# Kernel optimization log

Measured on AMD Instinct MI355X. Metric: run time of the kernel, lower is better.

The kernel has to match this reference:

```python
import jax, jax.numpy as jnp
import numpy as np


def setup_inputs() -> dict:
    key = jax.random.key(0)
    k1, _ = jax.random.split(key)
    x = jax.random.normal(k1, (8, 128, 56, 56), dtype=jnp.float32)
    gamma = jnp.array(0.5, dtype=jnp.float32)  # learned scalar (init gamma=0.5)
    return {"x": x, "gamma": gamma}


def reference(x, gamma):
    # conv=False path: query/key/value convs are Identity, so Q=K=V=x flattened.
    B, C, H, W = x.shape
    N = H * W
    v = x.reshape(B, C, N)                          # [B, C, N]
    # energy[b, i, j] = sum_c x[b, c, i] * x[b, c, j]  (Q^T K)
    energy = jnp.einsum('bci,bcj->bij', v, v)       # [B, N, N]
    # multiplicative mask: zero out the diagonal BEFORE softmax (not -inf)
    mask = 1.0 - jnp.eye(N, dtype=energy.dtype)
    attention = jax.nn.softmax(energy * mask, axis=-1)  # [B, N, N]
    # out = bmm(V, attention): out[b, c, j] = sum_i v[b, c, i] * attention[b, i, j]
    out = jnp.einsum('bci,bij->bcj', v, attention)  # [B, C, N]
    out = jax.nn.relu(out).reshape(B, C, H, W)
    y = gamma * out + x
    return (y, out, x, gamma)
```

## Files before the change

kernel.cpp:

```cpp
#include <hip/hip_runtime.h>
#include <math.h>

#define Bb 8
#define Cc 128
#define Nn 3136
#define Np 3200
#define NT 50
#define Mm (Bb*Cc*Nn)
#define PADV 72
#define L2E 1.44269504088896340736f
#define C44 (44.0f * L2E)

#define XT2B (NT*16*64*8)
#define XC2B (NT*8*128*8)

typedef unsigned short u16;
typedef unsigned int   u32;
typedef __attribute__((ext_vector_type(8)))  u16      u16x8;
typedef __attribute__((ext_vector_type(8)))  _Float16 f16x8;
typedef __attribute__((ext_vector_type(4)))  _Float16 f16x4;
typedef __attribute__((ext_vector_type(4)))  float    f32x4;
typedef __attribute__((ext_vector_type(16))) float    f32x16;

__device__ __forceinline__ float exp2fast(float x) {
#if __has_builtin(__builtin_amdgcn_exp2f)
    return __builtin_amdgcn_exp2f(x);
#else
    float r; asm("v_exp_f32 %0, %1" : "=v"(r) : "v"(x)); return r;
#endif
}

__global__ __launch_bounds__(256) void prep_kernel(const float* __restrict__ x,
                                                   const float* __restrict__ gamma_p,
                                                   float* __restrict__ out,
                                                   u16* __restrict__ xt2,
                                                   u16* __restrict__ xc2,
                                                   float* __restrict__ row_d) {
    const int bx = blockIdx.x;
    const int b = bx / 50, nblk = bx % 50;
    const int t = threadIdx.x;

    if (nblk == 49) {
        const u16x8 z8 = {0, 0, 0, 0, 0, 0, 0, 0};
        u16* dt = xt2 + ((size_t)b * NT + 49) * (16 * 64 * 8);
        u16* dc = xc2 + ((size_t)b * NT + 49) * (8 * 128 * 8);
        #pragma unroll
        for (int it = 0; it < 4; ++it) {
            *(u16x8*)&dt[(it * 256 + t) * 8] = z8;
            *(u16x8*)&dc[(it * 256 + t) * 8] = z8;
        }
        if (t < 64) row_d[b * Np + Nn + t] = 1.0f;
        return;
    }

    __shared__ float lx[Cc][65];
    const int n0 = nblk * 64;

    #pragma unroll 8
    for (int r = 0; r < 32; ++r) {
        const int c = r * 4 + (t >> 6);
        const int g = (b * Cc + c) * Nn + n0 + (t & 63);
        lx[c][t & 63] = x[g];
    }
    __syncthreads();

    {
        const int nl = t & 63, cseg = t >> 6;
        u16x8 hv[4];
        #pragma unroll
        for (int cc = 0; cc < 32; ++cc) {
            const _Float16 hh = (_Float16)lx[cseg * 32 + cc][nl];
            hv[cc >> 3][cc & 7] = __builtin_bit_cast(u16, hh);
        }
        u16* base = xt2 + (((size_t)(b * NT + nblk) * 16 + cseg * 4) * 64 + nl) * 8;
        #pragma unroll
        for (int k = 0; k < 4; ++k) *(u16x8*)&base[k * (64 * 8)] = hv[k];
    }
    {
        const int c = t >> 1, half = t & 1;
        u16x8 hv[4];
        #pragma unroll
        for (int k = 0; k < 32; ++k) {
            const _Float16 hh = (_Float16)lx[c][half * 32 + k];
            hv[k >> 3][k & 7] = __builtin_bit_cast(u16, hh);
        }
        u16* base = xc2 + (((size_t)(b * NT + nblk) * 8 + half * 4) * 128 + c) * 8;
        #pragma unroll
        for (int k = 0; k < 4; ++k) *(u16x8*)&base[k * (128 * 8)] = hv[k];
    }
    if (bx == 0 && t == 0) out[(size_t)3 * Mm] = gamma_p[0];
}

__global__ __launch_bounds__(256, 5) void stats_kernel(const u16* __restrict__ xt2,
                                                       float* __restrict__ row_d) {
    const int bx = blockIdx.x;
    const int b = bx & 7, rem = bx >> 3;
    const int i0t = rem >> 3, jq = rem & 7;
    const int t = threadIdx.x;
    const int w = t >> 6, l = t & 63, lane = l & 31, h = l >> 5;
    const int igrp = w & 1, jsub = w >> 1;
    const u16* __restrict__ xb = xt2 + (size_t)b * XT2B;

    f16x8 Bf[8];
    const int irow = igrp * 32 + lane;
    #pragma unroll
    for (int kk = 0; kk < 8; ++kk)
        Bf[kk] = *(const f16x8*)&xb[(((size_t)i0t * 16 + 2 * kk + h) * 64 + irow) * 8];

    const int jt0 = jq * 6 + (jq < 2 ? jq : 2);
    const int jcnt = 6 + (jq < 2 ? 1 : 0);
    const int jrow = jsub * 32 + lane;

    float sa = 0.f, sb = 0.f;
    for (int jt = jt0; jt < jt0 + jcnt; ++jt) {
        const u16* ab = &xb[((size_t)jt * 16 * 64 + jrow) * 8];
        f32x16 ea, eb;
        #pragma unroll
        for (int r = 0; r < 16; ++r) { ea[r] = 0.f; eb[r] = 0.f; }
        __builtin_amdgcn_s_setprio(1);
        #pragma unroll
        for (int kk = 0; kk < 4; ++kk) {
            const f16x8 A0 = *(const f16x8*)&ab[(4 * kk + h) * 512];
            const f16x8 A1 = *(const f16x8*)&ab[(4 * kk + 2 + h) * 512];
            ea = __builtin_amdgcn_mfma_f32_32x32x16_f16(A0, Bf[2 * kk],     ea, 0, 0, 0);
            eb = __builtin_amdgcn_mfma_f32_32x32x16_f16(A1, Bf[2 * kk + 1], eb, 0, 0, 0);
        }
        __builtin_amdgcn_s_setprio(0);

        if (jt == i0t) {
            const bool dsub = (jsub == igrp);
            #pragma unroll
            for (int r = 0; r < 16; ++r) {
                const int mrow = (r & 3) + 8 * (r >> 2) + 4 * h;
                float v = ea[r] + eb[r];
                if (dsub && mrow == lane) v = 0.f;
                const float e = exp2fast(fmaf(v, L2E, -C44));
                if (r & 1) sb += e; else sa += e;
            }
        } else {
            #pragma unroll
            for (int r = 0; r < 16; ++r) {
                const float e = exp2fast(fmaf(ea[r] + eb[r], L2E, -C44));
                if (r & 1) sb += e; else sa += e;
            }
        }
    }
    float ssum = sa + sb;
    ssum += __shfl_xor(ssum, 32, 64);
    if (h == 0) atomicAdd(&row_d[b * Np + i0t * 64 + igrp * 32 + lane], ssum);
}

__global__ __launch_bounds__(256) void conv_kernel(float* __restrict__ row_d) {
    const int i = blockIdx.x * 256 + threadIdx.x;
    row_d[i] = C44 + __log2f(row_d[i]);
}

__global__ __launch_bounds__(256, 3) void out_kernel(const u16* __restrict__ xt2,
                                                     const u16* __restrict__ xc2,
                                                     const float* __restrict__ row_c,
                                                     float* __restrict__ out) {
    __shared__ u16 s_pt[2][64 * PADV];

    const int bx = blockIdx.x;
    const int b = bx & 7, rem = bx >> 3;
    const int j0t = rem >> 1, ih = rem & 1;
    const int ti0 = ih * 25, ti1 = ti0 + 25;
    const int t = threadIdx.x;
    const int w = t >> 6, l = t & 63, lane = l & 31, h = l >> 5;
    const int isub = w & 1, jgrp = w >> 1;
    const int jg = w & 1,  cp = w >> 1;
    const u16* __restrict__ xtb = xt2 + (size_t)b * XT2B;
    const u16* __restrict__ xcb = xc2 + (size_t)b * XC2B;

    f16x8 Bj[8];
    const int jrow = jgrp * 32 + lane;
    #pragma unroll
    for (int kk = 0; kk < 8; ++kk)
        Bj[kk] = *(const f16x8*)&xtb[(((size_t)j0t * 16 + 2 * kk + h) * 64 + jrow) * 8];

    f32x16 oa, ob;
    #pragma unroll
    for (int r = 0; r < 16; ++r) { oa[r] = 0.f; ob[r] = 0.f; }

    const int arow = isub * 32 + lane;
    const int ptbase = (jgrp * 32 + lane) * PADV + isub * 32;
    const int pbrow = (jg * 32 + lane) * PADV + h * 8;

    f16x8 Ac[8];
    {
        const u16* ab = &xtb[((size_t)ti0 * 16 * 64 + arow) * 8];
        #pragma unroll
        for (int kk = 0; kk < 8; ++kk)
            Ac[kk] = *(const f16x8*)&ab[(2 * kk + h) * 512];
    }

    for (int ti = ti0; ti < ti1; ++ti) {
        const int tn = (ti + 1 < ti1) ? ti + 1 : ti;
        f16x8 An[8];
        const u16* abn = &xtb[((size_t)tn * 16 * 64 + arow) * 8];
        #pragma unroll
        for (int kk = 0; kk < 8; ++kk)
            An[kk] = *(const f16x8*)&abn[(2 * kk + h) * 512];

        f32x16 ea;
        #pragma unroll
        for (int r = 0; r < 16; ++r) ea[r] = 0.f;
        #pragma unroll
        for (int kk = 0; kk < 8; ++kk)
            ea = __builtin_amdgcn_mfma_f32_32x32x16_f16(Ac[kk], Bj[kk], ea, 0, 0, 0);

        u16* pt = &s_pt[ti & 1][0];
        const float* cbase = &row_c[b * Np + ti * 64 + isub * 32];
        if (ti == j0t) {
            const bool dsub = (isub == jgrp);
            #pragma unroll
            for (int qq = 0; qq < 4; ++qq) {
                const f32x4 cv = *(const f32x4*)&cbase[qq * 8 + h * 4];
                f16x4 pv;
                #pragma unroll
                for (int r = 0; r < 4; ++r) {
                    const int m = qq * 8 + h * 4 + r;
                    float v = ea[qq * 4 + r];
                    if (dsub && m == lane) v = 0.f;
                    pv[r] = (_Float16)exp2fast(fmaf(v, L2E, -cv[r]));
                }
                *(f16x4*)&pt[ptbase + qq * 8 + h * 4] = pv;
            }
        } else {
            #pragma unroll
            for (int qq = 0; qq < 4; ++qq) {
                const f32x4 cv = *(const f32x4*)&cbase[qq * 8 + h * 4];
                f16x4 pv;
                #pragma unroll
                for (int r = 0; r < 4; ++r)
                    pv[r] = (_Float16)exp2fast(fmaf(ea[qq * 4 + r], L2E, -cv[r]));
                *(f16x4*)&pt[ptbase + qq * 8 + h * 4] = pv;
            }
        }

        f16x8 Av[4][2];
        const u16* vb = &xcb[((size_t)ti * 8 * 128 + cp * 64 + lane) * 8];
        #pragma unroll
        for (int kk = 0; kk < 4; ++kk) {
            Av[kk][0] = *(const f16x8*)&vb[((2 * kk + h) * 128) * 8];
            Av[kk][1] = *(const f16x8*)&vb[((2 * kk + h) * 128 + 32) * 8];
        }
        __syncthreads();

        #pragma unroll
        for (int kk = 0; kk < 4; ++kk) {
            const f16x8 Bp = *(const f16x8*)&pt[pbrow + kk * 16];
            oa = __builtin_amdgcn_mfma_f32_32x32x16_f16(Av[kk][0], Bp, oa, 0, 0, 0);
            ob = __builtin_amdgcn_mfma_f32_32x32x16_f16(Av[kk][1], Bp, ob, 0, 0, 0);
        }

        #pragma unroll
        for (int kk = 0; kk < 8; ++kk) Ac[kk] = An[kk];
    }

    #pragma unroll
    for (int r = 0; r < 16; ++r) {
        const int mrow = (r & 3) + 8 * (r >> 2) + 4 * h;
        const int jj = j0t * 64 + jg * 32 + lane;
        {
            const int c = cp * 64 + mrow;
            const size_t pos = (size_t)(b * Cc + c) * Nn + jj;
            out[(size_t)ih * Mm + pos] = oa[r];
        }
        {
            const int c = cp * 64 + 32 + mrow;
            const size_t pos = (size_t)(b * Cc + c) * Nn + jj;
            out[(size_t)ih * Mm + pos] = ob[r];
        }
    }
}

__global__ __launch_bounds__(256) void finish_kernel(const float* __restrict__ x,
                                                     const float* __restrict__ gamma_p,
                                                     float* __restrict__ out) {
    const float gamma = gamma_p[0];
    const size_t base = ((size_t)blockIdx.x * 256 + threadIdx.x) * 4;
    const f32x4 pa = *(const f32x4*)&out[base];
    const f32x4 pb = *(const f32x4*)&out[(size_t)Mm + base];
    const f32x4 xv = *(const f32x4*)&x[base];
    f32x4 yo, oo;
    #pragma unroll
    for (int r = 0; r < 4; ++r) {
        const float o = fmaxf(pa[r] + pb[r], 0.0f);
        oo[r] = o;
        yo[r] = fmaf(gamma, o, xv[r]);
    }
    *(f32x4*)&out[base] = yo;
    *(f32x4*)&out[(size_t)Mm + base] = oo;
    *(f32x4*)&out[(size_t)2 * Mm + base] = xv;
}

extern "C" void kernel_launch(void* const* d_in, const int* in_sizes, int n_in,
                              void* d_out, int out_size, void* d_ws, size_t ws_size,
                              hipStream_t stream) {
    const float* x       = (const float*)d_in[0];
    const float* gamma_p = (const float*)d_in[1];
    float* out = (float*)d_out;

    float* row_d = (float*)d_ws;
    u16* xt2 = (u16*)((char*)d_ws + (1 << 17));
    u16* xc2 = xt2 + (size_t)Bb * XT2B;

    hipMemsetAsync(row_d, 0, (size_t)Bb * Np * sizeof(float), stream);
    prep_kernel  <<<400, 256, 0, stream>>>(x, gamma_p, out, xt2, xc2, row_d);
    stats_kernel <<<3136, 256, 0, stream>>>(xt2, row_d);
    conv_kernel  <<<100, 256, 0, stream>>>(row_d);
    out_kernel   <<<784, 256, 0, stream>>>(xt2, xc2, row_d, out);
    finish_kernel<<<3136, 256, 0, stream>>>(x, gamma_p, out);
}
```

Baseline: 195.6 us.

## Stage key/value tiles in LDS via async global_load_lds double buffering

Both the stats and out kernels now copy each upcoming key tile (and, in out_kernel, the value tile) into double-buffered shared memory with direct global-to-LDS loads, and feed the MFMAs from LDS instead of per-wave global/register loads. Previously each wave re-read the same tile from global memory into registers. The aim is to cut redundant global traffic and register pressure and to overlap the next tile's load with the current compute. In exchange it uses more LDS, lowers occupancy hints (5→4 and 3→2 blocks per CU), adds an extra barrier per iteration, and single-buffers the P tile, adding synchronization.

```diff
diff --git a/kernel.cpp b/kernel.cpp
--- a/kernel.cpp
+++ b/kernel.cpp
@@ -12,7 +12,9 @@
 #define C44 (44.0f * L2E)
 
 #define XT2B (NT*16*64*8)
+#define TSZA (16*64*8)
 #define XC2B (NT*8*128*8)
+#define TSZV (8*128*8)
 
 typedef unsigned short u16;
 typedef unsigned int   u32;
@@ -28,6 +30,12 @@
 #else
     float r; asm("v_exp_f32 %0, %1" : "=v"(r) : "v"(x)); return r;
 #endif
+}
+
+typedef __attribute__((address_space(1))) const unsigned int gas_u32;
+typedef __attribute__((address_space(3))) unsigned int las_u32;
+__device__ __forceinline__ void gload_lds16(const u16* g, u16* l) {
+    __builtin_amdgcn_global_load_lds((gas_u32*)g, (las_u32*)l, 16, 0, 0);
 }
 
 __global__ __launch_bounds__(256) void prep_kernel(const float* __restrict__ x,
@@ -42,8 +50,8 @@
 
     if (nblk == 49) {
         const u16x8 z8 = {0, 0, 0, 0, 0, 0, 0, 0};
-        u16* dt = xt2 + ((size_t)b * NT + 49) * (16 * 64 * 8);
-        u16* dc = xc2 + ((size_t)b * NT + 49) * (8 * 128 * 8);
+        u16* dt = xt2 + ((size_t)b * NT + 49) * TSZA;
+        u16* dc = xc2 + ((size_t)b * NT + 49) * TSZV;
         #pragma unroll
         for (int it = 0; it < 4; ++it) {
             *(u16x8*)&dt[(it * 256 + t) * 8] = z8;
@@ -91,8 +99,10 @@
     if (bx == 0 && t == 0) out[(size_t)3 * Mm] = gamma_p[0];
 }
 
-__global__ __launch_bounds__(256, 5) void stats_kernel(const u16* __restrict__ xt2,
+__global__ __launch_bounds__(256, 4) void stats_kernel(const u16* __restrict__ xt2,
                                                        float* __restrict__ row_d) {
+    __shared__ __align__(16) u16 s_j[2][TSZA];
+
     const int bx = blockIdx.x;
     const int b = bx & 7, rem = bx >> 3;
     const int i0t = rem >> 3, jq = rem & 7;
@@ -110,18 +120,35 @@
     const int jt0 = jq * 6 + (jq < 2 ? jq : 2);
     const int jcnt = 6 + (jq < 2 ? 1 : 0);
     const int jrow = jsub * 32 + lane;
+    const int wsh = w * 2048;
+
+    {
+        const u16* gs = xb + (size_t)jt0 * TSZA + wsh + l * 8;
+        u16* ls = &s_j[0][wsh];
+        #pragma unroll
+        for (int k = 0; k < 4; ++k) gload_lds16(gs + k * 512, ls + k * 512);
+    }
+    __syncthreads();
 
     float sa = 0.f, sb = 0.f;
     for (int jt = jt0; jt < jt0 + jcnt; ++jt) {
-        const u16* ab = &xb[((size_t)jt * 16 * 64 + jrow) * 8];
+        const int cur = (jt - jt0) & 1;
+        if (jt + 1 < jt0 + jcnt) {
+            const u16* gs = xb + (size_t)(jt + 1) * TSZA + wsh + l * 8;
+            u16* ls = &s_j[cur ^ 1][wsh];
+            #pragma unroll
+            for (int k = 0; k < 4; ++k) gload_lds16(gs + k * 512, ls + k * 512);
+        }
+
+        const u16* sj = &s_j[cur][0];
         f32x16 ea, eb;
         #pragma unroll
         for (int r = 0; r < 16; ++r) { ea[r] = 0.f; eb[r] = 0.f; }
         __builtin_amdgcn_s_setprio(1);
         #pragma unroll
         for (int kk = 0; kk < 4; ++kk) {
-            const f16x8 A0 = *(const f16x8*)&ab[(4 * kk + h) * 512];
-            const f16x8 A1 = *(const f16x8*)&ab[(4 * kk + 2 + h) * 512];
+            const f16x8 A0 = *(const f16x8*)&sj[((4 * kk + h) * 64 + jrow) * 8];
+            const f16x8 A1 = *(const f16x8*)&sj[((4 * kk + 2 + h) * 64 + jrow) * 8];
             ea = __builtin_amdgcn_mfma_f32_32x32x16_f16(A0, Bf[2 * kk],     ea, 0, 0, 0);
             eb = __builtin_amdgcn_mfma_f32_32x32x16_f16(A1, Bf[2 * kk + 1], eb, 0, 0, 0);
         }
@@ -144,6 +171,7 @@
                 if (r & 1) sb += e; else sa += e;
             }
         }
+        __syncthreads();
     }
     float ssum = sa + sb;
     ssum += __shfl_xor(ssum, 32, 64);
@@ -155,11 +183,13 @@
     row_d[i] = C44 + __log2f(row_d[i]);
 }
 
-__global__ __launch_bounds__(256, 3) void out_kernel(const u16* __restrict__ xt2,
+__global__ __launch_bounds__(256, 2) void out_kernel(const u16* __restrict__ xt2,
                                                      const u16* __restrict__ xc2,
                                                      const float* __restrict__ row_c,
                                                      float* __restrict__ out) {
-    __shared__ u16 s_pt[2][64 * PADV];
+    __shared__ __align__(16) u16 s_xa[2][TSZA];
+    __shared__ __align__(16) u16 s_xv[2][TSZV];
+    __shared__ __align__(16) u16 s_pt[64 * PADV];
 
     const int bx = blockIdx.x;
     const int b = bx & 7, rem = bx >> 3;
@@ -186,30 +216,40 @@
     const int ptbase = (jgrp * 32 + lane) * PADV + isub * 32;
     const int pbrow = (jg * 32 + lane) * PADV + h * 8;
 
-    f16x8 Ac[8];
+    const bool wA = (w < 2);
+    const int sh = (w & 1) * 4096;
+
     {
-        const u16* ab = &xtb[((size_t)ti0 * 16 * 64 + arow) * 8];
-        #pragma unroll
-        for (int kk = 0; kk < 8; ++kk)
-            Ac[kk] = *(const f16x8*)&ab[(2 * kk + h) * 512];
-    }
+        const u16* gs = (wA ? xtb + (size_t)ti0 * TSZA : xcb + (size_t)ti0 * TSZV)
+                        + sh + l * 8;
+        u16* ls = (wA ? &s_xa[0][0] : &s_xv[0][0]) + sh;
+        #pragma unroll
+        for (int k = 0; k < 8; ++k) gload_lds16(gs + k * 512, ls + k * 512);
+    }
+    __syncthreads();
 
     for (int ti = ti0; ti < ti1; ++ti) {
-        const int tn = (ti + 1 < ti1) ? ti + 1 : ti;
-        f16x8 An[8];
-        const u16* abn = &xtb[((size_t)tn * 16 * 64 + arow) * 8];
-        #pragma unroll
-        for (int kk = 0; kk < 8; ++kk)
-            An[kk] = *(const f16x8*)&abn[(2 * kk + h) * 512];
-
+        const int cur = (ti - ti0) & 1;
+        if (ti + 1 < ti1) {
+            const u16* gs = (wA ? xtb + (size_t)(ti + 1) * TSZA
+                                : xcb + (size_t)(ti + 1) * TSZV) + sh + l * 8;
+            u16* ls = (wA ? &s_xa[cur ^ 1][0] : &s_xv[cur ^ 1][0]) + sh;
+            #pragma unroll
+            for (int k = 0; k < 8; ++k) gload_lds16(gs + k * 512, ls + k * 512);
+        }
+
+        const u16* sa = &s_xa[cur][0];
         f32x16 ea;
         #pragma unroll
         for (int r = 0; r < 16; ++r) ea[r] = 0.f;
-        #pragma unroll
-        for (int kk = 0; kk < 8; ++kk)
-            ea = __builtin_amdgcn_mfma_f32_32x32x16_f16(Ac[kk], Bj[kk], ea, 0, 0, 0);
-
-        u16* pt = &s_pt[ti & 1][0];
+        __builtin_amdgcn_s_setprio(1);
+        #pragma unroll
+        for (int kk = 0; kk < 8; ++kk) {
+            const f16x8 A = *(const f16x8*)&sa[((2 * kk + h) * 64 + arow) * 8];
+            ea = __builtin_amdgcn_mfma_f32_32x32x16_f16(A, Bj[kk], ea, 0, 0, 0);
+        }
+        __builtin_amdgcn_s_setprio(0);
+
         const float* cbase = &row_c[b * Np + ti * 64 + isub * 32];
         if (ti == j0t) {
             const bool dsub = (isub == jgrp);
@@ -224,7 +264,7 @@
                     if (dsub && m == lane) v = 0.f;
                     pv[r] = (_Float16)exp2fast(fmaf(v, L2E, -cv[r]));
                 }
-                *(f16x4*)&pt[ptbase + qq * 8 + h * 4] = pv;
+                *(f16x4*)&s_pt[ptbase + qq * 8 + h * 4] = pv;
             }
         } else {
             #pragma unroll
@@ -234,28 +274,23 @@
                 #pragma unroll
                 for (int r = 0; r < 4; ++r)
                     pv[r] = (_Float16)exp2fast(fmaf(ea[qq * 4 + r], L2E, -cv[r]));
-                *(f16x4*)&pt[ptbase + qq * 8 + h * 4] = pv;
+                *(f16x4*)&s_pt[ptbase + qq * 8 + h * 4] = pv;
             }
         }
-
-        f16x8 Av[4][2];
-        const u16* vb = &xcb[((size_t)ti * 8 * 128 + cp * 64 + lane) * 8];
+        __syncthreads();
+
+        const u16* sv = &s_xv[cur][0];
+        __builtin_amdgcn_s_setprio(1);
         #pragma unroll
         for (int kk = 0; kk < 4; ++kk) {
-            Av[kk][0] = *(const f16x8*)&vb[((2 * kk + h) * 128) * 8];
-            Av[kk][1] = *(const f16x8*)&vb[((2 * kk + h) * 128 + 32) * 8];
-        }
+            const f16x8 Bp  = *(const f16x8*)&s_pt[pbrow + kk * 16];
+            const f16x8 Av0 = *(const f16x8*)&sv[((2 * kk + h) * 128 + cp * 64 + lane) * 8];
+            const f16x8 Av1 = *(const f16x8*)&sv[((2 * kk + h) * 128 + cp * 64 + 32 + lane) * 8];
+            oa = __builtin_amdgcn_mfma_f32_32x32x16_f16(Av0, Bp, oa, 0, 0, 0);
+            ob = __builtin_amdgcn_mfma_f32_32x32x16_f16(Av1, Bp, ob, 0, 0, 0);
+        }
+        __builtin_amdgcn_s_setprio(0);
         __syncthreads();
-
-        #pragma unroll
-        for (int kk = 0; kk < 4; ++kk) {
-            const f16x8 Bp = *(const f16x8*)&pt[pbrow + kk * 16];
-            oa = __builtin_amdgcn_mfma_f32_32x32x16_f16(Av[kk][0], Bp, oa, 0, 0, 0);
-            ob = __builtin_amdgcn_mfma_f32_32x32x16_f16(Av[kk][1], Bp, ob, 0, 0, 0);
-        }
-
-        #pragma unroll
-        for (int kk = 0; kk < 8; ++kk) Ac[kk] = An[kk];
     }
 
     #pragma unroll
```

Measured after the change: 191.6 us. -2.1%, faster.

## Materialize quantized energy matrix once instead of recomputing QK^T in output pass

Applied to the files above, without the earlier changes.

A new e_kernel computes each energy tile once, accumulates the softmax denominators, and stores the energies as 16-bit fixed-point (scaled by 256) in workspace. A pv_kernel then streams those tiles into LDS with async global-to-LDS loads, dequantizes them, applies exp and multiplies by V. This removes the second QK^T GEMM that the old output kernel repeated. In exchange it adds heavy memory traffic for the N×N energy buffer and quantization error in the energies. Depending on workspace size it processes batches in chunks and falls back to the old path when the workspace is too small.

```diff
diff --git a/kernel.cpp b/kernel.cpp
--- a/kernel.cpp
+++ b/kernel.cpp
@@ -6,19 +6,26 @@
 #define Nn 3136
 #define Np 3200
 #define NT 50
+#define NRT 49
 #define Mm (Bb*Cc*Nn)
 #define PADV 72
 #define L2E 1.44269504088896340736f
 #define C44 (44.0f * L2E)
+#define ESCL 256.0f
+#define KDEC (L2E / 256.0f)
 
 #define XT2B (NT*16*64*8)
 #define XC2B (NT*8*128*8)
+#define ETILE 4096
+#define EBATCH ((size_t)NRT*NRT*ETILE)
+#define WS_BASE (131072 + 2*(size_t)Bb*XT2B*2)
 
 typedef unsigned short u16;
 typedef unsigned int   u32;
 typedef __attribute__((ext_vector_type(8)))  u16      u16x8;
 typedef __attribute__((ext_vector_type(8)))  _Float16 f16x8;
 typedef __attribute__((ext_vector_type(4)))  _Float16 f16x4;
+typedef __attribute__((ext_vector_type(4)))  u32      u32x4;
 typedef __attribute__((ext_vector_type(4)))  float    f32x4;
 typedef __attribute__((ext_vector_type(16))) float    f32x16;
 
@@ -28,6 +35,21 @@
 #else
     float r; asm("v_exp_f32 %0, %1" : "=v"(r) : "v"(x)); return r;
 #endif
+}
+
+typedef __attribute__((address_space(1))) const unsigned int gas_u32;
+typedef __attribute__((address_space(3))) unsigned int las_u32;
+__device__ __forceinline__ void gload_lds16(const u16* g, u16* l) {
+    __builtin_amdgcn_global_load_lds((gas_u32*)g, (las_u32*)l, 16, 0, 0);
+}
+
+#define BAR()    __builtin_amdgcn_s_barrier()
+#define SCHED0() __builtin_amdgcn_sched_barrier(0)
+#define W_ALL()  asm volatile("s_waitcnt vmcnt(0) lgkmcnt(0)" ::: "memory")
+
+__device__ __forceinline__ u32 pack_i16(float a, float b) {
+    const int qa = (int)a, qb = (int)b;
+    return (u32)(qa & 0xffff) | ((u32)qb << 16);
 }
 
 __global__ __launch_bounds__(256) void prep_kernel(const float* __restrict__ x,
@@ -91,7 +113,189 @@
     if (bx == 0 && t == 0) out[(size_t)3 * Mm] = gamma_p[0];
 }
 
-__global__ __launch_bounds__(256, 5) void stats_kernel(const u16* __restrict__ xt2,
+__global__ __launch_bounds__(256, 4) void e_kernel(const u16* __restrict__ xt2,
+                                                   u16* __restrict__ E,
+                                                   float* __restrict__ row_d,
+                                                   int bofs, int nb) {
+    const int bx = blockIdx.x;
+    const int b_ = bx % nb, rem = bx / nb;
+    const int jt = rem >> 2, iq = rem & 3;
+    const int b = bofs + b_;
+    const int t = threadIdx.x;
+    const int w = t >> 6, l = t & 63, lane = l & 31, h = l >> 5;
+    const int isub = w & 1, jgrp = w >> 1;
+    const u16* __restrict__ xb = xt2 + (size_t)b * XT2B;
+
+    f16x8 Bj[8];
+    const int jrow = jgrp * 32 + lane;
+    #pragma unroll
+    for (int kk = 0; kk < 8; ++kk)
+        Bj[kk] = *(const f16x8*)&xb[(((size_t)jt * 16 + 2 * kk + h) * 64 + jrow) * 8];
+
+    const int it0 = iq * 12 + (iq ? 1 : 0);
+    const int icnt = iq ? 12 : 13;
+    const int arow = isub * 32 + lane;
+
+    float dA = 0.f, dB = 0.f;
+    for (int it = it0; it < it0 + icnt; ++it) {
+        const u16* ab = &xb[((size_t)it * 16 * 64 + arow) * 8];
+        f32x16 ea;
+        #pragma unroll
+        for (int r = 0; r < 16; ++r) ea[r] = 0.f;
+        __builtin_amdgcn_s_setprio(1);
+        #pragma unroll
+        for (int kk = 0; kk < 8; ++kk) {
+            const f16x8 A = *(const f16x8*)&ab[(2 * kk + h) * 512];
+            ea = __builtin_amdgcn_mfma_f32_32x32x16_f16(A, Bj[kk], ea, 0, 0, 0);
+        }
+        __builtin_amdgcn_s_setprio(0);
+
+        const bool dt = (it == jt) && (isub == jgrp);
+        u32 pk[4][2], sw[4][2];
+        #pragma unroll
+        for (int qq = 0; qq < 4; ++qq) {
+            float pv[4];
+            #pragma unroll
+            for (int r2 = 0; r2 < 4; ++r2) {
+                const int m = qq * 8 + h * 4 + r2;
+                float v = ea[qq * 4 + r2];
+                if (dt && m == lane) v = 0.f;
+                pv[r2] = v;
+                const float e = exp2fast(fmaf(v, L2E, -C44));
+                if (r2 & 1) dB += e; else dA += e;
+            }
+            pk[qq][0] = pack_i16(pv[0] * ESCL, pv[1] * ESCL);
+            pk[qq][1] = pack_i16(pv[2] * ESCL, pv[3] * ESCL);
+            sw[qq][0] = __shfl_xor(pk[qq][0], 32, 64);
+            sw[qq][1] = __shfl_xor(pk[qq][1], 32, 64);
+        }
+        u16* eb = E + ((((size_t)(b_ * NRT + jt) * NRT + it) * 2 + jgrp) * 4) * 512;
+        #pragma unroll
+        for (int kt = 0; kt < 2; ++kt) {
+            u32x4 bw;
+            bw[0] = h ? sw[2 * kt + 1][0] : pk[2 * kt][0];
+            bw[1] = h ? sw[2 * kt + 1][1] : pk[2 * kt][1];
+            bw[2] = h ? pk[2 * kt + 1][0] : sw[2 * kt][0];
+            bw[3] = h ? pk[2 * kt + 1][1] : sw[2 * kt][1];
+            *(u32x4*)&eb[(isub * 2 + kt) * 512 + l * 8] = bw;
+        }
+    }
+    float d = dA + dB;
+    d += __shfl_xor(d, 32, 64);
+    if (h == 0) atomicAdd(&row_d[b * Np + jt * 64 + jgrp * 32 + lane], d);
+}
+
+__global__ __launch_bounds__(256) void conv_kernel(float* __restrict__ row_d) {
+    const int i = blockIdx.x * 256 + threadIdx.x;
+    row_d[i] = C44 + __log2f(row_d[i]);
+}
+
+__global__ __launch_bounds__(256, 3) void pv_kernel(const u16* __restrict__ xc2,
+                                                    const u16* __restrict__ E,
+                                                    const float* __restrict__ row_c,
+                                                    float* __restrict__ out,
+                                                    int bofs, int nb) {
+    __shared__ __align__(16) u16 s_e[2][ETILE];
+
+    const int bx = blockIdx.x;
+    const int b_ = bx % nb, rem = bx / nb;
+    const int jt = rem >> 1, kh = rem & 1;
+    const int b = bofs + b_;
+    const int it0 = kh ? 25 : 0, it1 = kh ? 49 : 25;
+    const int t = threadIdx.x;
+    const int w = t >> 6, l = t & 63, lane = l & 31, h = l >> 5;
+    const int jg = w & 1, cp = w >> 1;
+    const u16* __restrict__ xcb = xc2 + (size_t)b * XC2B;
+    const u16* __restrict__ Eb = E + (size_t)(b_ * NRT + jt) * NRT * ETILE;
+
+    f32x16 a0, a1;
+    #pragma unroll
+    for (int r = 0; r < 16; ++r) { a0[r] = 0.f; a1[r] = 0.f; }
+
+    {
+        const u16* gs = Eb + (size_t)it0 * ETILE + (w * 2) * 512 + l * 8;
+        u16* ls = &s_e[0][(w * 2) * 512];
+        gload_lds16(gs, ls);
+        gload_lds16(gs + 512, ls + 512);
+    }
+    W_ALL(); BAR(); SCHED0();
+
+    for (int it = it0; it < it1; ++it) {
+        const int cur = (it - it0) & 1;
+        if (it + 1 < it1) {
+            const u16* gs = Eb + (size_t)(it + 1) * ETILE + (w * 2) * 512 + l * 8;
+            u16* ls = &s_e[cur ^ 1][(w * 2) * 512];
+            gload_lds16(gs, ls);
+            gload_lds16(gs + 512, ls + 512);
+        }
+
+        const float* cb = &row_c[b * Np + it * 64];
+        f16x8 Bp[4];
+        #pragma unroll
+        for (int s = 0; s < 4; ++s) {
+            const u16x8 ev = *(const u16x8*)&s_e[cur][(jg * 4 + s) * 512 + l * 8];
+            const f32x4 cA = *(const f32x4*)&cb[s * 16 + h * 8];
+            const f32x4 cB = *(const f32x4*)&cb[s * 16 + h * 8 + 4];
+            float p[8];
+            #pragma unroll
+            for (int e = 0; e < 8; ++e) {
+                const float f = (float)(short)ev[e];
+                const float c = (e < 4) ? cA[e] : cB[e - 4];
+                p[e] = exp2fast(fmaf(f, KDEC, -c));
+            }
+            u32x4 bw;
+            bw[0] = __builtin_bit_cast(u32, __builtin_amdgcn_cvt_pkrtz(p[0], p[1]));
+            bw[1] = __builtin_bit_cast(u32, __builtin_amdgcn_cvt_pkrtz(p[2], p[3]));
+            bw[2] = __builtin_bit_cast(u32, __builtin_amdgcn_cvt_pkrtz(p[4], p[5]));
+            bw[3] = __builtin_bit_cast(u32, __builtin_amdgcn_cvt_pkrtz(p[6], p[7]));
+            Bp[s] = __builtin_bit_cast(f16x8, bw);
+        }
+
+        __builtin_amdgcn_s_setprio(1);
+        #pragma unroll
+        for (int s = 0; s < 4; ++s) {
+            const f16x8 Av0 = *(const f16x8*)&xcb[((size_t)(it * 8 + s * 2 + h) * 128 + cp * 64 + lane) * 8];
+            const f16x8 Av1 = *(const f16x8*)&xcb[((size_t)(it * 8 + s * 2 + h) * 128 + cp * 64 + 32 + lane) * 8];
+            a0 = __builtin_amdgcn_mfma_f32_32x32x16_f16(Av0, Bp[s], a0, 0, 0, 0);
+            a1 = __builtin_amdgcn_mfma_f32_32x32x16_f16(Av1, Bp[s], a1, 0, 0, 0);
+        }
+        __builtin_amdgcn_s_setprio(0);
+
+        W_ALL(); BAR(); SCHED0();
+    }
+
+    #pragma unroll
+    for (int r = 0; r < 16; ++r) {
+        const int mrow = (r & 3) + 8 * (r >> 2) + 4 * h;
+        const int jj = jt * 64 + jg * 32 + lane;
+        const size_t p0 = (size_t)(b * Cc + cp * 64 + mrow) * Nn + jj;
+        const size_t p1 = (size_t)(b * Cc + cp * 64 + 32 + mrow) * Nn + jj;
+        out[(size_t)kh * Mm + p0] = a0[r];
+        out[(size_t)kh * Mm + p1] = a1[r];
+    }
+}
+
+__global__ __launch_bounds__(256) void finish_kernel(const float* __restrict__ x,
+                                                     const float* __restrict__ gamma_p,
+                                                     float* __restrict__ out) {
+    const float gamma = gamma_p[0];
+    const size_t base = ((size_t)blockIdx.x * 256 + threadIdx.x) * 4;
+    const f32x4 pa = *(const f32x4*)&out[base];
+    const f32x4 pb = *(const f32x4*)&out[(size_t)Mm + base];
+    const f32x4 xv = *(const f32x4*)&x[base];
+    f32x4 yo, oo;
+    #pragma unroll
+    for (int r = 0; r < 4; ++r) {
+        const float o = fmaxf(pa[r] + pb[r], 0.0f);
+        oo[r] = o;
+        yo[r] = fmaf(gamma, o, xv[r]);
+    }
+    *(f32x4*)&out[base] = yo;
+    *(f32x4*)&out[(size_t)Mm + base] = oo;
+    *(f32x4*)&out[(size_t)2 * Mm + base] = xv;
+}
+
+__global__ __launch_bounds__(256, 5) void stats_legacy(const u16* __restrict__ xt2,
                                                        float* __restrict__ row_d) {
     const int bx = blockIdx.x;
     const int b = bx & 7, rem = bx >> 3;
@@ -117,7 +321,6 @@
         f32x16 ea, eb;
         #pragma unroll
         for (int r = 0; r < 16; ++r) { ea[r] = 0.f; eb[r] = 0.f; }
-        __builtin_amdgcn_s_setprio(1);
         #pragma unroll
         for (int kk = 0; kk < 4; ++kk) {
             const f16x8 A0 = *(const f16x8*)&ab[(4 * kk + h) * 512];
@@ -125,24 +328,14 @@
             ea = __builtin_amdgcn_mfma_f32_32x32x16_f16(A0, Bf[2 * kk],     ea, 0, 0, 0);
             eb = __builtin_amdgcn_mfma_f32_32x32x16_f16(A1, Bf[2 * kk + 1], eb, 0, 0, 0);
         }
-        __builtin_amdgcn_s_setprio(0);
-
-        if (jt == i0t) {
-            const bool dsub = (jsub == igrp);
-            #pragma unroll
-            for (int r = 0; r < 16; ++r) {
-                const int mrow = (r & 3) + 8 * (r >> 2) + 4 * h;
-                float v = ea[r] + eb[r];
-                if (dsub && mrow == lane) v = 0.f;
-                const float e = exp2fast(fmaf(v, L2E, -C44));
-                if (r & 1) sb += e; else sa += e;
-            }
-        } else {
-            #pragma unroll
-            for (int r = 0; r < 16; ++r) {
-                const float e = exp2fast(fmaf(ea[r] + eb[r], L2E, -C44));
-                if (r & 1) sb += e; else sa += e;
-            }
+        const bool diag = (jt == i0t) && (jsub == igrp);
+        #pragma unroll
+        for (int r = 0; r < 16; ++r) {
+            const int mrow = (r & 3) + 8 * (r >> 2) + 4 * h;
+            float v = ea[r] + eb[r];
+            if (diag && mrow == lane) v = 0.f;
+            const float e = exp2fast(fmaf(v, L2E, -C44));
+            if (r & 1) sb += e; else sa += e;
         }
     }
     float ssum = sa + sb;
@@ -150,12 +343,7 @@
     if (h == 0) atomicAdd(&row_d[b * Np + i0t * 64 + igrp * 32 + lane], ssum);
 }
 
-__global__ __launch_bounds__(256) void conv_kernel(float* __restrict__ row_d) {
-    const int i = blockIdx.x * 256 + threadIdx.x;
-    row_d[i] = C44 + __log2f(row_d[i]);
-}
-
-__global__ __launch_bounds__(256, 3) void out_kernel(const u16* __restrict__ xt2,
+__global__ __launch_bounds__(256, 3) void out_legacy(const u16* __restrict__ xt2,
                                                      const u16* __restrict__ xc2,
                                                      const float* __restrict__ row_c,
                                                      float* __restrict__ out) {
@@ -211,31 +399,19 @@
 
         u16* pt = &s_pt[ti & 1][0];
         const float* cbase = &row_c[b * Np + ti * 64 + isub * 32];
-        if (ti == j0t) {
-            const bool dsub = (isub == jgrp);
+        const bool dsub = (ti == j0t) && (isub == jgrp);
+        #pragma unroll
+        for (int qq = 0; qq < 4; ++qq) {
+            const f32x4 cv = *(const f32x4*)&cbase[qq * 8 + h * 4];
+            f16x4 pv;
             #pragma unroll
-            for (int qq = 0; qq < 4; ++qq) {
-                const f32x4 cv = *(const f32x4*)&cbase[qq * 8 + h * 4];
-                f16x4 pv;
-                #pragma unroll
-                for (int r = 0; r < 4; ++r) {
-                    const int m = qq * 8 + h * 4 + r;
-                    float v = ea[qq * 4 + r];
-                    if (dsub && m == lane) v = 0.f;
-                    pv[r] = (_Float16)exp2fast(fmaf(v, L2E, -cv[r]));
-                }
-                *(f16x4*)&pt[ptbase + qq * 8 + h * 4] = pv;
+            for (int r = 0; r < 4; ++r) {
+                const int m = qq * 8 + h * 4 + r;
+                float v = ea[qq * 4 + r];
+                if (dsub && m == lane) v = 0.f;
+                pv[r] = (_Float16)exp2fast(fmaf(v, L2E, -cv[r]));
             }
-        } else {
-            #pragma unroll
-            for (int qq = 0; qq < 4; ++qq) {
-                const f32x4 cv = *(const f32x4*)&cbase[qq * 8 + h * 4];
-                f16x4 pv;
-                #pragma unroll
-                for (int r = 0; r < 4; ++r)
-                    pv[r] = (_Float16)exp2fast(fmaf(ea[qq * 4 + r], L2E, -cv[r]));
-                *(f16x4*)&pt[ptbase + qq * 8 + h * 4] = pv;
-            }
+            *(f16x4*)&pt[ptbase + qq * 8 + h * 4] = pv;
         }
 
         f16x8 Av[4][2];
@@ -253,7 +429,6 @@
             oa = __builtin_amdgcn_mfma_f32_32x32x16_f16(Av[kk][0], Bp, oa, 0, 0, 0);
             ob = __builtin_amdgcn_mfma_f32_32x32x16_f16(Av[kk][1], Bp, ob, 0, 0, 0);
         }
-
         #pragma unroll
         for (int kk = 0; kk < 8; ++kk) Ac[kk] = An[kk];
     }
@@ -262,37 +437,11 @@
     for (int r = 0; r < 16; ++r) {
         const int mrow = (r & 3) + 8 * (r >> 2) + 4 * h;
         const int jj = j0t * 64 + jg * 32 + lane;
-        {
-            const int c = cp * 64 + mrow;
-            const size_t pos = (size_t)(b * Cc + c) * Nn + jj;
-            out[(size_t)ih * Mm + pos] = oa[r];
-        }
-        {
-            const int c = cp * 64 + 32 + mrow;
-            const size_t pos = (size_t)(b * Cc + c) * Nn + jj;
-            out[(size_t)ih * Mm + pos] = ob[r];
-        }
-    }
-}
-
-__global__ __launch_bounds__(256) void finish_kernel(const float* __restrict__ x,
-                                                     const float* __restrict__ gamma_p,
-                                                     float* __restrict__ out) {
-    const float gamma = gamma_p[0];
-    const size_t base = ((size_t)blockIdx.x * 256 + threadIdx.x) * 4;
-    const f32x4 pa = *(const f32x4*)&out[base];
-    const f32x4 pb = *(const f32x4*)&out[(size_t)Mm + base];
-    const f32x4 xv = *(const f32x4*)&x[base];
-    f32x4 yo, oo;
-    #pragma unroll
-    for (int r = 0; r < 4; ++r) {
-        const float o = fmaxf(pa[r] + pb[r], 0.0f);
-        oo[r] = o;
-        yo[r] = fmaf(gamma, o, xv[r]);
-    }
-    *(f32x4*)&out[base] = yo;
-    *(f32x4*)&out[(size_t)Mm + base] = oo;
-    *(f32x4*)&out[(size_t)2 * Mm + base] = xv;
+        const size_t p0 = (size_t)(b * Cc + cp * 64 + mrow) * Nn + jj;
+        const size_t p1 = (size_t)(b * Cc + cp * 64 + 32 + mrow) * Nn + jj;
+        out[(size_t)ih * Mm + p0] = oa[r];
+        out[(size_t)ih * Mm + p1] = ob[r];
+    }
 }
 
 extern "C" void kernel_launch(void* const* d_in, const int* in_sizes, int n_in,
@@ -305,11 +454,27 @@
     float* row_d = (float*)d_ws;
     u16* xt2 = (u16*)((char*)d_ws + (1 << 17));
     u16* xc2 = xt2 + (size_t)Bb * XT2B;
+    u16* E   = (u16*)((char*)d_ws + WS_BASE);
+    const size_t ebytes1 = EBATCH * 2;
 
     hipMemsetAsync(row_d, 0, (size_t)Bb * Np * sizeof(float), stream);
-    prep_kernel  <<<400, 256, 0, stream>>>(x, gamma_p, out, xt2, xc2, row_d);
-    stats_kernel <<<3136, 256, 0, stream>>>(xt2, row_d);
-    conv_kernel  <<<100, 256, 0, stream>>>(row_d);
-    out_kernel   <<<784, 256, 0, stream>>>(xt2, xc2, row_d, out);
+    prep_kernel<<<400, 256, 0, stream>>>(x, gamma_p, out, xt2, xc2, row_d);
+
+    int nb = 0;
+    if      (ws_size >= WS_BASE + 8 * ebytes1) nb = 8;
+    else if (ws_size >= WS_BASE + 4 * ebytes1) nb = 4;
+    else if (ws_size >= WS_BASE + 2 * ebytes1) nb = 2;
+
+    if (nb) {
+        for (int bofs = 0; bofs < Bb; bofs += nb) {
+            e_kernel <<<nb * 196, 256, 0, stream>>>(xt2, E, row_d, bofs, nb);
+            conv_kernel<<<(nb * Np) / 256, 256, 0, stream>>>(row_d + (size_t)bofs * Np);
+            pv_kernel<<<nb * 98, 256, 0, stream>>>(xc2, E, row_d, out, bofs, nb);
+        }
+    } else {
+        stats_legacy<<<3136, 256, 0, stream>>>(xt2, row_d);
+        conv_kernel <<<100, 256, 0, stream>>>(row_d);
+        out_legacy  <<<784, 256, 0, stream>>>(xt2, xc2, row_d, out);
+    }
     finish_kernel<<<3136, 256, 0, stream>>>(x, gamma_p, out);
 }
```

Measured after the change: 198.3 us. No clear change (+1.4%).
